# Kernel optimization log

Hardware: AMD Instinct MI355X
Metric: run time of the kernel (lower is better)

The kernel has to match this reference:

```python
import jax, jax.numpy as jnp
import numpy as np

B, E, T, H = 4, 16, 1024, 1024
NEG = -10000.0


def setup_inputs() -> dict:
    key = jax.random.key(0)
    ks = jax.random.split(key, 9)
    s = 1.0 / np.sqrt(H)
    return {
        "token_embedding": jax.random.normal(ks[0], (B, T, H), jnp.float32),
        "entity_embedding": jax.random.normal(ks[1], (B, E, H), jnp.float32),
        "token_mask": jax.random.bernoulli(ks[2], 0.9, (B, T)),
        "Wt": jax.random.normal(ks[3], (H, H), jnp.float32) * s,
        "bt": jax.random.normal(ks[4], (H,), jnp.float32) * s,
        "We": jax.random.normal(ks[5], (H, H), jnp.float32) * s,
        "be": jax.random.normal(ks[6], (H,), jnp.float32) * s,
        "Wp": jax.random.normal(ks[7], (H,), jnp.float32) * s,
        "bp": jax.random.normal(ks[8], (1,), jnp.float32) * s,
    }


def reference(token_embedding, entity_embedding, token_mask, Wt, bt, We, be, Wp, bp):
    # token branch: [B,T,H] @ [H,H] -> [B,T,H]
    t = jnp.einsum('bth,hk->btk', token_embedding, Wt) + bt
    # entity branch: [B,E,H] @ [H,H] -> [B,E,H]
    e = jnp.einsum('beh,hk->bek', entity_embedding, We) + be
    # broadcast add -> relu -> linear-to-scalar: [B,E,T,H] -> [B,E,T]
    m = jax.nn.relu(t[:, None, :, :] + e[:, :, None, :])
    cls = jnp.einsum('beth,h->bet', m, Wp) + bp[0]
    # mask fill (after squeeze, per squeeze=True path)
    cls = jnp.where(token_mask[:, None, :], cls, NEG)
    p = jax.nn.sigmoid(cls)
    return cls, p
```

## Files before the change

### kernel.cpp

```cpp
#include <hip/hip_runtime.h>

typedef unsigned short us;
typedef __attribute__((ext_vector_type(8))) short short8;
typedef __attribute__((ext_vector_type(4))) float f32x4;

__device__ __forceinline__ us f2bf(float f) {
  unsigned int u = __builtin_bit_cast(unsigned int, f);
  u += 0x7fffu + ((u >> 16) & 1u);
  return (us)(u >> 16);
}

__device__ __forceinline__ void gload_lds16(const void* g, void* l) {
  __builtin_amdgcn_global_load_lds(
      (const __attribute__((address_space(1))) void*)g,
      (__attribute__((address_space(3))) void*)l, 16, 0, 0);
}

__global__ __launch_bounds__(256) void prep_kernel(
    const float* __restrict__ token, us* __restrict__ tokb,
    const float* __restrict__ Wt, us* __restrict__ WtT,
    const float* __restrict__ entity, const float* __restrict__ We,
    float* __restrict__ epart) {
  __shared__ float tile[64][65];
  __shared__ float eS[16][128];
  const int bid = blockIdx.x, tid = threadIdx.x;
  if (bid < 256) {
    int kc = bid & 7, nt = (bid >> 3) & 7, b = bid >> 6;
    int k0 = kc << 7, n0 = nt << 7;
#pragma unroll
    for (int p = 0; p < 2; ++p) {
      int idx = (p << 8) + tid;
      int r = idx >> 5, kk = (idx & 31) << 2;
      *(float4*)&eS[r][kk] = *(const float4*)&entity[(size_t)(((b << 4) + r) << 10) + k0 + kk];
    }
    __syncthreads();
    const int col = tid & 127, rh = tid >> 7;
    const float* wP = We + ((size_t)k0 << 10) + n0 + col;
    float acc[8] = {0.f, 0.f, 0.f, 0.f, 0.f, 0.f, 0.f, 0.f};
#pragma unroll 8
    for (int k = 0; k < 128; ++k) {
      float wv = wP[(size_t)k << 10];
#pragma unroll
      for (int r = 0; r < 8; ++r)
        acc[r] = fmaf(wv, eS[(rh << 3) + r][k], acc[r]);
    }
    float* op = epart + (((size_t)((kc << 6) + (b << 4) + (rh << 3))) << 10) + n0 + col;
#pragma unroll
    for (int r = 0; r < 8; ++r) op[(size_t)r << 10] = acc[r];
  } else if (bid < 4352) {
    int q = (bid - 256) * 256 + tid;
    float4 v = ((const float4*)token)[q];
    ushort4 o;
    o.x = f2bf(v.x); o.y = f2bf(v.y); o.z = f2bf(v.z); o.w = f2bf(v.w);
    ((ushort4*)tokb)[q] = o;
  } else {
    int tb = bid - 4352;
    int bx = (tb & 15) << 6, by = ((tb >> 4) & 15) << 6;
    int r0 = tid >> 4, c0 = (tid & 15) << 2;
#pragma unroll
    for (int p = 0; p < 4; ++p) {
      int r = p * 16 + r0;
      float4 v = *(const float4*)&Wt[(size_t)(by + r) * 1024 + bx + c0];
      tile[r][c0] = v.x; tile[r][c0 + 1] = v.y;
      tile[r][c0 + 2] = v.z; tile[r][c0 + 3] = v.w;
    }
    __syncthreads();
#pragma unroll
    for (int p = 0; p < 4; ++p) {
      int r = p * 16 + r0;
      ushort4 o;
      o.x = f2bf(tile[c0 + 0][r]); o.y = f2bf(tile[c0 + 1][r]);
      o.z = f2bf(tile[c0 + 2][r]); o.w = f2bf(tile[c0 + 3][r]);
      *(ushort4*)&WtT[(size_t)(bx + r) * 1024 + by + c0] = o;
    }
  }
}

__global__ __launch_bounds__(256) void main_kernel(
    const us* __restrict__ tokb, const us* __restrict__ WtT,
    const float* __restrict__ epart, const float* __restrict__ be,
    const float* __restrict__ bt, const float* __restrict__ wp,
    float* __restrict__ partial) {
  __shared__ __attribute__((aligned(16))) us Ws[2][4096];
  __shared__ __attribute__((aligned(16))) us Ts[2][2048];
  __shared__ __attribute__((aligned(16))) float eL[16][132];
  __shared__ __attribute__((aligned(16))) float btL[128];
  __shared__ __attribute__((aligned(16))) float wpL[128];
  __shared__ float pp[2][64][17];
  const int tid = threadIdx.x;
  const int mh = blockIdx.x, tt = blockIdx.y;
  const int h0 = mh << 7, b = tt >> 4, t0 = (tt & 15) << 6;
#pragma unroll
  for (int p = 0; p < 2; ++p) {
    int q = (p << 8) + tid;
    int er = q >> 5, ec = (q & 31) << 2;
    f32x4 s = *(const f32x4*)&be[h0 + ec];
#pragma unroll
    for (int kc = 0; kc < 8; ++kc)
      s += *(const f32x4*)&epart[(((size_t)((kc << 6) + (b << 4) + er)) << 10) + h0 + ec];
    *(f32x4*)&eL[er][ec] = s;
  }
  if (tid < 128) btL[tid] = bt[h0 + tid];
  else wpL[tid - 128] = wp[h0 + tid - 128];
  asm volatile("" ::: "memory");
  const int row1 = tid >> 2, kc4 = (tid & 3) << 3;
  const us* wP = WtT + (size_t)(h0 + row1) * 1024 + kc4;
  const us* tP = tokb + (size_t)((b << 10) + t0 + row1) * 1024 + kc4;
  const int w = tid >> 6;
  us* w0 = &Ws[0][w * 512]; us* w1 = &Ws[1][w * 512];
  us* t0L = &Ts[0][w * 512]; us* t1L = &Ts[1][w * 512];
  gload_lds16(wP, w0); gload_lds16(wP + 65536, w0 + 2048);
  gload_lds16(tP, t0L);
  gload_lds16(wP + 32, w1); gload_lds16(wP + 65536 + 32, w1 + 2048);
  gload_lds16(tP + 32, t1L);
  const int lane = tid & 63, wm = (tid >> 7) & 1, wn = (tid >> 6) & 1;
  const int l16 = lane & 15, oct = lane >> 4, ko = oct << 3;
  int wfo[4], tfo[2];
#pragma unroll
  for (int i = 0; i < 4; ++i) wfo[i] = (((wm << 6) + (i << 4) + l16) << 5) + ko;
#pragma unroll
  for (int j = 0; j < 2; ++j) tfo[j] = (((wn << 5) + (j << 4) + l16) << 5) + ko;
  f32x4 acc[4][2] = {};
  for (int kt = 0; kt < 32; ++kt) {
    const us* Wb = Ws[kt & 1];
    const us* Tb = Ts[kt & 1];
    __builtin_amdgcn_s_waitcnt(0x0f73);
    __builtin_amdgcn_s_barrier();
    asm volatile("" ::: "memory");
    short8 af[4], bfr[2];
#pragma unroll
    for (int i = 0; i < 4; ++i) af[i] = *(const short8*)&Wb[wfo[i]];
#pragma unroll
    for (int j = 0; j < 2; ++j) bfr[j] = *(const short8*)&Tb[tfo[j]];
#pragma unroll
    for (int i = 0; i < 4; ++i)
#pragma unroll
      for (int j = 0; j < 2; ++j)
        acc[i][j] = __builtin_amdgcn_mfma_f32_16x16x32_bf16(af[i], bfr[j], acc[i][j], 0, 0, 0);
    asm volatile("" ::: "memory");
    __builtin_amdgcn_s_barrier();
    int nk = kt + 2; if (nk > 31) nk = 30;
    int ko2 = nk << 5;
    us* dw = (kt & 1) ? w1 : w0;
    us* dt = (kt & 1) ? t1L : t0L;
    gload_lds16(wP + ko2, dw); gload_lds16(wP + 65536 + ko2, dw + 2048);
    gload_lds16(tP + ko2, dt);
  }
  f32x4 btq[4], wpq[4];
#pragma unroll
  for (int i = 0; i < 4; ++i) {
    int hb = (wm << 6) + (i << 4) + (oct << 2);
    btq[i] = *(const f32x4*)&btL[hb];
    wpq[i] = *(const f32x4*)&wpL[hb];
  }
#pragma unroll
  for (int i = 0; i < 4; ++i)
#pragma unroll
    for (int j = 0; j < 2; ++j) acc[i][j] += btq[i];
#pragma unroll
  for (int e = 0; e < 16; ++e) {
    f32x4 ev[4];
#pragma unroll
    for (int i = 0; i < 4; ++i)
      ev[i] = *(const f32x4*)&eL[e][(wm << 6) + (i << 4) + (oct << 2)];
    float pj[2] = {0.f, 0.f};
#pragma unroll
    for (int j = 0; j < 2; ++j)
#pragma unroll
      for (int i = 0; i < 4; ++i)
#pragma unroll
        for (int r = 0; r < 4; ++r)
          pj[j] = fmaf(fmaxf(acc[i][j][r] + ev[i][r], 0.f), wpq[i][r], pj[j]);
#pragma unroll
    for (int j = 0; j < 2; ++j) {
      pj[j] += __shfl_xor(pj[j], 16, 64);
      pj[j] += __shfl_xor(pj[j], 32, 64);
    }
    if (oct == 0) {
#pragma unroll
      for (int j = 0; j < 2; ++j) pp[wm][(wn << 5) + (j << 4) + l16][e] = pj[j];
    }
  }
  __syncthreads();
#pragma unroll
  for (int q = 0; q < 4; ++q) {
    int flat = (q << 8) + tid;
    int e = flat >> 6, tl = flat & 63;
    float v = pp[0][tl][e] + pp[1][tl][e];
    partial[((size_t)mh << 16) + (size_t)((((b << 4) + e) << 10) + t0 + tl)] = v;
  }
}

__global__ __launch_bounds__(256) void finalize_kernel(
    const float* __restrict__ partial, const float* __restrict__ bp,
    const int* __restrict__ mask, float* __restrict__ out) {
  int idx = blockIdx.x * 256 + threadIdx.x;
  float s = 0.f;
#pragma unroll
  for (int mh = 0; mh < 8; ++mh) s += partial[((size_t)mh << 16) + idx];
  float cls = s + bp[0];
  int b = idx >> 14, t = idx & 1023;
  if (mask[(b << 10) + t] == 0) cls = -10000.0f;
  float p = 1.0f / (1.0f + __expf(-cls));
  out[idx] = cls;
  out[65536 + idx] = p;
}

extern "C" void kernel_launch(void* const* d_in, const int* in_sizes, int n_in,
                              void* d_out, int out_size, void* d_ws, size_t ws_size,
                              hipStream_t stream) {
  const float* token = (const float*)d_in[0];
  const float* entity = (const float*)d_in[1];
  const int* mask = (const int*)d_in[2];
  const float* Wt = (const float*)d_in[3];
  const float* bt = (const float*)d_in[4];
  const float* We = (const float*)d_in[5];
  const float* be = (const float*)d_in[6];
  const float* Wp = (const float*)d_in[7];
  const float* bp = (const float*)d_in[8];
  float* out = (float*)d_out;

  char* ws = (char*)d_ws;
  us* tokb = (us*)ws;
  us* WtT = tokb + (size_t)4096 * 1024;
  float* epart = (float*)(WtT + (size_t)1024 * 1024);
  float* partial = epart + (size_t)8 * 64 * 1024;

  prep_kernel<<<4608, 256, 0, stream>>>(token, tokb, Wt, WtT, entity, We, epart);
  main_kernel<<<dim3(8, 64), 256, 0, stream>>>(tokb, WtT, epart, be, bt, Wp, partial);
  finalize_kernel<<<256, 256, 0, stream>>>(partial, bp, mask, out);
}
```

Before: 114.0 us.

## Triple-buffer GEMM LDS pipeline and issue prefetch before epilogue setup

Moves the main kernel's K-loop from double to triple buffering, so each tile's global-to-LDS load is issued three steps ahead, and the wait count is relaxed to allow more loads in flight. The first three prefetches are issued before the entity and bias setup so that setup overlaps the memory latency. The epilogue now runs in two halves of eight entities to shrink the partial-sum shared buffer, at the cost of one extra barrier. More LDS per block may reduce occupancy.

```diff
diff --git a/kernel.cpp b/kernel.cpp
--- a/kernel.cpp
+++ b/kernel.cpp
@@ -81,15 +81,27 @@
     const float* __restrict__ epart, const float* __restrict__ be,
     const float* __restrict__ bt, const float* __restrict__ wp,
     float* __restrict__ partial) {
-  __shared__ __attribute__((aligned(16))) us Ws[2][4096];
-  __shared__ __attribute__((aligned(16))) us Ts[2][2048];
+  __shared__ __attribute__((aligned(16))) us Ws[3][4096];
+  __shared__ __attribute__((aligned(16))) us Ts[3][2048];
   __shared__ __attribute__((aligned(16))) float eL[16][132];
   __shared__ __attribute__((aligned(16))) float btL[128];
   __shared__ __attribute__((aligned(16))) float wpL[128];
-  __shared__ float pp[2][64][17];
+  __shared__ float pp[2][64][9];
   const int tid = threadIdx.x;
   const int mh = blockIdx.x, tt = blockIdx.y;
   const int h0 = mh << 7, b = tt >> 4, t0 = (tt & 15) << 6;
+  const int row1 = tid >> 2, kc4 = (tid & 3) << 3;
+  const us* wP = WtT + (size_t)(h0 + row1) * 1024 + kc4;
+  const us* tP = tokb + (size_t)((b << 10) + t0 + row1) * 1024 + kc4;
+  const int w = tid >> 6;
+  us* wB[3] = {&Ws[0][w * 512], &Ws[1][w * 512], &Ws[2][w * 512]};
+  us* tB[3] = {&Ts[0][w * 512], &Ts[1][w * 512], &Ts[2][w * 512]};
+#pragma unroll
+  for (int j = 0; j < 3; ++j) {
+    gload_lds16(wP + (j << 5), wB[j]);
+    gload_lds16(wP + 65536 + (j << 5), wB[j] + 2048);
+    gload_lds16(tP + (j << 5), tB[j]);
+  }
 #pragma unroll
   for (int p = 0; p < 2; ++p) {
     int q = (p << 8) + tid;
@@ -103,16 +115,6 @@
   if (tid < 128) btL[tid] = bt[h0 + tid];
   else wpL[tid - 128] = wp[h0 + tid - 128];
   asm volatile("" ::: "memory");
-  const int row1 = tid >> 2, kc4 = (tid & 3) << 3;
-  const us* wP = WtT + (size_t)(h0 + row1) * 1024 + kc4;
-  const us* tP = tokb + (size_t)((b << 10) + t0 + row1) * 1024 + kc4;
-  const int w = tid >> 6;
-  us* w0 = &Ws[0][w * 512]; us* w1 = &Ws[1][w * 512];
-  us* t0L = &Ts[0][w * 512]; us* t1L = &Ts[1][w * 512];
-  gload_lds16(wP, w0); gload_lds16(wP + 65536, w0 + 2048);
-  gload_lds16(tP, t0L);
-  gload_lds16(wP + 32, w1); gload_lds16(wP + 65536 + 32, w1 + 2048);
-  gload_lds16(tP + 32, t1L);
   const int lane = tid & 63, wm = (tid >> 7) & 1, wn = (tid >> 6) & 1;
   const int l16 = lane & 15, oct = lane >> 4, ko = oct << 3;
   int wfo[4], tfo[2];
@@ -121,31 +123,39 @@
 #pragma unroll
   for (int j = 0; j < 2; ++j) tfo[j] = (((wn << 5) + (j << 4) + l16) << 5) + ko;
   f32x4 acc[4][2] = {};
-  for (int kt = 0; kt < 32; ++kt) {
-    const us* Wb = Ws[kt & 1];
-    const us* Tb = Ts[kt & 1];
-    __builtin_amdgcn_s_waitcnt(0x0f73);
-    __builtin_amdgcn_s_barrier();
-    asm volatile("" ::: "memory");
-    short8 af[4], bfr[2];
-#pragma unroll
-    for (int i = 0; i < 4; ++i) af[i] = *(const short8*)&Wb[wfo[i]];
-#pragma unroll
-    for (int j = 0; j < 2; ++j) bfr[j] = *(const short8*)&Tb[tfo[j]];
-#pragma unroll
-    for (int i = 0; i < 4; ++i)
-#pragma unroll
-      for (int j = 0; j < 2; ++j)
-        acc[i][j] = __builtin_amdgcn_mfma_f32_16x16x32_bf16(af[i], bfr[j], acc[i][j], 0, 0, 0);
-    asm volatile("" ::: "memory");
-    __builtin_amdgcn_s_barrier();
-    int nk = kt + 2; if (nk > 31) nk = 30;
-    int ko2 = nk << 5;
-    us* dw = (kt & 1) ? w1 : w0;
-    us* dt = (kt & 1) ? t1L : t0L;
-    gload_lds16(wP + ko2, dw); gload_lds16(wP + 65536 + ko2, dw + 2048);
-    gload_lds16(tP + ko2, dt);
-  }
+#define KBODY(KT, BUF, VMC, ISSUE)                                              \
+  {                                                                             \
+    __builtin_amdgcn_s_waitcnt(VMC);                                            \
+    __builtin_amdgcn_s_barrier();                                               \
+    asm volatile("" ::: "memory");                                              \
+    short8 af[4], bfr[2];                                                       \
+    _Pragma("unroll") for (int i = 0; i < 4; ++i)                               \
+        af[i] = *(const short8*)&Ws[BUF][wfo[i]];                               \
+    _Pragma("unroll") for (int j = 0; j < 2; ++j)                               \
+        bfr[j] = *(const short8*)&Ts[BUF][tfo[j]];                              \
+    _Pragma("unroll") for (int i = 0; i < 4; ++i)                               \
+        _Pragma("unroll") for (int j = 0; j < 2; ++j)                           \
+            acc[i][j] = __builtin_amdgcn_mfma_f32_16x16x32_bf16(                \
+                af[i], bfr[j], acc[i][j], 0, 0, 0);                             \
+    asm volatile("" ::: "memory");                                              \
+    if (ISSUE) {                                                                \
+      __builtin_amdgcn_s_barrier();                                             \
+      int nk = (KT) + 3; if (nk > 31) nk = 31;  \
+      int ko2 = nk << 5;                                                        \
+      gload_lds16(wP + ko2, wB[BUF]);                                           \
+      gload_lds16(wP + 65536 + ko2, wB[BUF] + 2048);                            \
+      gload_lds16(tP + ko2, tB[BUF]);                                           \
+    }                                                                           \
+  }
+  for (int g = 0; g < 10; ++g) {
+    int kt = g * 3;
+    KBODY(kt + 0, 0, 0x0f76, 1);
+    KBODY(kt + 1, 1, 0x0f76, 1);
+    KBODY(kt + 2, 2, 0x0f76, 1);
+  }
+  KBODY(30, 0, 0x0f76, 0);
+  KBODY(31, 1, 0x0f73, 0);
+#undef KBODY
   f32x4 btq[4], wpq[4];
 #pragma unroll
   for (int i = 0; i < 4; ++i) {
@@ -157,37 +167,42 @@
   for (int i = 0; i < 4; ++i)
 #pragma unroll
     for (int j = 0; j < 2; ++j) acc[i][j] += btq[i];
-#pragma unroll
-  for (int e = 0; e < 16; ++e) {
-    f32x4 ev[4];
-#pragma unroll
-    for (int i = 0; i < 4; ++i)
-      ev[i] = *(const f32x4*)&eL[e][(wm << 6) + (i << 4) + (oct << 2)];
-    float pj[2] = {0.f, 0.f};
-#pragma unroll
-    for (int j = 0; j < 2; ++j)
+  for (int eh = 0; eh < 2; ++eh) {
+    __syncthreads();
+#pragma unroll
+    for (int e8 = 0; e8 < 8; ++e8) {
+      int e = (eh << 3) + e8;
+      f32x4 ev[4];
 #pragma unroll
       for (int i = 0; i < 4; ++i)
-#pragma unroll
-        for (int r = 0; r < 4; ++r)
-          pj[j] = fmaf(fmaxf(acc[i][j][r] + ev[i][r], 0.f), wpq[i][r], pj[j]);
-#pragma unroll
-    for (int j = 0; j < 2; ++j) {
-      pj[j] += __shfl_xor(pj[j], 16, 64);
-      pj[j] += __shfl_xor(pj[j], 32, 64);
-    }
-    if (oct == 0) {
-#pragma unroll
-      for (int j = 0; j < 2; ++j) pp[wm][(wn << 5) + (j << 4) + l16][e] = pj[j];
-    }
-  }
-  __syncthreads();
-#pragma unroll
-  for (int q = 0; q < 4; ++q) {
-    int flat = (q << 8) + tid;
-    int e = flat >> 6, tl = flat & 63;
-    float v = pp[0][tl][e] + pp[1][tl][e];
-    partial[((size_t)mh << 16) + (size_t)((((b << 4) + e) << 10) + t0 + tl)] = v;
+        ev[i] = *(const f32x4*)&eL[e][(wm << 6) + (i << 4) + (oct << 2)];
+      float pj[2] = {0.f, 0.f};
+#pragma unroll
+      for (int j = 0; j < 2; ++j)
+#pragma unroll
+        for (int i = 0; i < 4; ++i)
+#pragma unroll
+          for (int r = 0; r < 4; ++r)
+            pj[j] = fmaf(fmaxf(acc[i][j][r] + ev[i][r], 0.f), wpq[i][r], pj[j]);
+#pragma unroll
+      for (int j = 0; j < 2; ++j) {
+        pj[j] += __shfl_xor(pj[j], 16, 64);
+        pj[j] += __shfl_xor(pj[j], 32, 64);
+      }
+      if (oct == 0) {
+#pragma unroll
+        for (int j = 0; j < 2; ++j) pp[wm][(wn << 5) + (j << 4) + l16][e8] = pj[j];
+      }
+    }
+    __syncthreads();
+#pragma unroll
+    for (int q = 0; q < 2; ++q) {
+      int flat = (q << 8) + tid;
+      int e8 = flat >> 6, tl = flat & 63;
+      float v = pp[0][tl][e8] + pp[1][tl][e8];
+      partial[((size_t)mh << 16) +
+              (size_t)((((b << 4) + (eh << 3) + e8) << 10) + t0 + tl)] = v;
+    }
   }
 }
 
```

Result: no change. 114.9 us (+0.8%).

## Fuse finalize into main kernel via atomic counter, load GEMM operands directly

Applied to the files above, without the earlier changes.

Removes the finalize kernel launch: each main-kernel block increments a per-token-tile counter, and the last of the 8 hidden-slice blocks sums the partials and writes cls and sigmoid outputs. The LDS double-buffered global_load_lds pipeline is replaced by direct per-lane global loads of MFMA fragments, with no per-step barriers. The grid is transposed and the pp scratch halved to 8 entities per pass. This saves a launch and the barrier overhead, but it gives up LDS staging and coalesced tile loads, so global load efficiency and latency hiding may suffer.

```diff
diff --git a/kernel.cpp b/kernel.cpp
--- a/kernel.cpp
+++ b/kernel.cpp
@@ -10,20 +10,15 @@
   return (us)(u >> 16);
 }
 
-__device__ __forceinline__ void gload_lds16(const void* g, void* l) {
-  __builtin_amdgcn_global_load_lds(
-      (const __attribute__((address_space(1))) void*)g,
-      (__attribute__((address_space(3))) void*)l, 16, 0, 0);
-}
-
 __global__ __launch_bounds__(256) void prep_kernel(
     const float* __restrict__ token, us* __restrict__ tokb,
     const float* __restrict__ Wt, us* __restrict__ WtT,
     const float* __restrict__ entity, const float* __restrict__ We,
-    float* __restrict__ epart) {
+    float* __restrict__ epart, int* __restrict__ cnt) {
   __shared__ float tile[64][65];
   __shared__ float eS[16][128];
   const int bid = blockIdx.x, tid = threadIdx.x;
+  if (bid == 0 && tid < 64) cnt[tid] = 0;
   if (bid < 256) {
     int kc = bid & 7, nt = (bid >> 3) & 7, b = bid >> 6;
     int k0 = kc << 7, n0 = nt << 7;
@@ -80,15 +75,16 @@
     const us* __restrict__ tokb, const us* __restrict__ WtT,
     const float* __restrict__ epart, const float* __restrict__ be,
     const float* __restrict__ bt, const float* __restrict__ wp,
-    float* __restrict__ partial) {
-  __shared__ __attribute__((aligned(16))) us Ws[2][4096];
-  __shared__ __attribute__((aligned(16))) us Ts[2][2048];
+    const float* __restrict__ bp, const int* __restrict__ mask,
+    float* __restrict__ partial, int* __restrict__ cnt,
+    float* __restrict__ out) {
   __shared__ __attribute__((aligned(16))) float eL[16][132];
   __shared__ __attribute__((aligned(16))) float btL[128];
   __shared__ __attribute__((aligned(16))) float wpL[128];
-  __shared__ float pp[2][64][17];
+  __shared__ float pp[2][64][9];
+  __shared__ int doneFlag;
   const int tid = threadIdx.x;
-  const int mh = blockIdx.x, tt = blockIdx.y;
+  const int tt = blockIdx.x, mh = blockIdx.y;
   const int h0 = mh << 7, b = tt >> 4, t0 = (tt & 15) << 6;
 #pragma unroll
   for (int p = 0; p < 2; ++p) {
@@ -102,50 +98,32 @@
   }
   if (tid < 128) btL[tid] = bt[h0 + tid];
   else wpL[tid - 128] = wp[h0 + tid - 128];
-  asm volatile("" ::: "memory");
-  const int row1 = tid >> 2, kc4 = (tid & 3) << 3;
-  const us* wP = WtT + (size_t)(h0 + row1) * 1024 + kc4;
-  const us* tP = tokb + (size_t)((b << 10) + t0 + row1) * 1024 + kc4;
-  const int w = tid >> 6;
-  us* w0 = &Ws[0][w * 512]; us* w1 = &Ws[1][w * 512];
-  us* t0L = &Ts[0][w * 512]; us* t1L = &Ts[1][w * 512];
-  gload_lds16(wP, w0); gload_lds16(wP + 65536, w0 + 2048);
-  gload_lds16(tP, t0L);
-  gload_lds16(wP + 32, w1); gload_lds16(wP + 65536 + 32, w1 + 2048);
-  gload_lds16(tP + 32, t1L);
   const int lane = tid & 63, wm = (tid >> 7) & 1, wn = (tid >> 6) & 1;
-  const int l16 = lane & 15, oct = lane >> 4, ko = oct << 3;
-  int wfo[4], tfo[2];
-#pragma unroll
-  for (int i = 0; i < 4; ++i) wfo[i] = (((wm << 6) + (i << 4) + l16) << 5) + ko;
-#pragma unroll
-  for (int j = 0; j < 2; ++j) tfo[j] = (((wn << 5) + (j << 4) + l16) << 5) + ko;
+  const int l16 = lane & 15, oct = lane >> 4;
+  const us* aP[4];
+  const us* bP[2];
+#pragma unroll
+  for (int i = 0; i < 4; ++i)
+    aP[i] = WtT + (size_t)(h0 + (wm << 6) + (i << 4) + l16) * 1024 + (oct << 3);
+#pragma unroll
+  for (int j = 0; j < 2; ++j)
+    bP[j] = tokb + (size_t)((b << 10) + t0 + (wn << 5) + (j << 4) + l16) * 1024 + (oct << 3);
   f32x4 acc[4][2] = {};
+#pragma unroll 4
   for (int kt = 0; kt < 32; ++kt) {
-    const us* Wb = Ws[kt & 1];
-    const us* Tb = Ts[kt & 1];
-    __builtin_amdgcn_s_waitcnt(0x0f73);
-    __builtin_amdgcn_s_barrier();
-    asm volatile("" ::: "memory");
+    const int ko = kt << 5;
     short8 af[4], bfr[2];
 #pragma unroll
-    for (int i = 0; i < 4; ++i) af[i] = *(const short8*)&Wb[wfo[i]];
-#pragma unroll
-    for (int j = 0; j < 2; ++j) bfr[j] = *(const short8*)&Tb[tfo[j]];
+    for (int i = 0; i < 4; ++i) af[i] = *(const short8*)(aP[i] + ko);
+#pragma unroll
+    for (int j = 0; j < 2; ++j) bfr[j] = *(const short8*)(bP[j] + ko);
 #pragma unroll
     for (int i = 0; i < 4; ++i)
 #pragma unroll
       for (int j = 0; j < 2; ++j)
         acc[i][j] = __builtin_amdgcn_mfma_f32_16x16x32_bf16(af[i], bfr[j], acc[i][j], 0, 0, 0);
-    asm volatile("" ::: "memory");
-    __builtin_amdgcn_s_barrier();
-    int nk = kt + 2; if (nk > 31) nk = 30;
-    int ko2 = nk << 5;
-    us* dw = (kt & 1) ? w1 : w0;
-    us* dt = (kt & 1) ? t1L : t0L;
-    gload_lds16(wP + ko2, dw); gload_lds16(wP + 65536 + ko2, dw + 2048);
-    gload_lds16(tP + ko2, dt);
-  }
+  }
+  __syncthreads();
   f32x4 btq[4], wpq[4];
 #pragma unroll
   for (int i = 0; i < 4; ++i) {
@@ -157,53 +135,66 @@
   for (int i = 0; i < 4; ++i)
 #pragma unroll
     for (int j = 0; j < 2; ++j) acc[i][j] += btq[i];
-#pragma unroll
-  for (int e = 0; e < 16; ++e) {
-    f32x4 ev[4];
-#pragma unroll
-    for (int i = 0; i < 4; ++i)
-      ev[i] = *(const f32x4*)&eL[e][(wm << 6) + (i << 4) + (oct << 2)];
-    float pj[2] = {0.f, 0.f};
-#pragma unroll
-    for (int j = 0; j < 2; ++j)
+  for (int eh = 0; eh < 2; ++eh) {
+    __syncthreads();
+#pragma unroll
+    for (int e8 = 0; e8 < 8; ++e8) {
+      int e = (eh << 3) + e8;
+      f32x4 ev[4];
 #pragma unroll
       for (int i = 0; i < 4; ++i)
-#pragma unroll
-        for (int r = 0; r < 4; ++r)
-          pj[j] = fmaf(fmaxf(acc[i][j][r] + ev[i][r], 0.f), wpq[i][r], pj[j]);
-#pragma unroll
-    for (int j = 0; j < 2; ++j) {
-      pj[j] += __shfl_xor(pj[j], 16, 64);
-      pj[j] += __shfl_xor(pj[j], 32, 64);
-    }
-    if (oct == 0) {
-#pragma unroll
-      for (int j = 0; j < 2; ++j) pp[wm][(wn << 5) + (j << 4) + l16][e] = pj[j];
-    }
+        ev[i] = *(const f32x4*)&eL[e][(wm << 6) + (i << 4) + (oct << 2)];
+      float pj[2] = {0.f, 0.f};
+#pragma unroll
+      for (int j = 0; j < 2; ++j)
+#pragma unroll
+        for (int i = 0; i < 4; ++i)
+#pragma unroll
+          for (int r = 0; r < 4; ++r)
+            pj[j] = fmaf(fmaxf(acc[i][j][r] + ev[i][r], 0.f), wpq[i][r], pj[j]);
+#pragma unroll
+      for (int j = 0; j < 2; ++j) {
+        pj[j] += __shfl_xor(pj[j], 16, 64);
+        pj[j] += __shfl_xor(pj[j], 32, 64);
+      }
+      if (oct == 0) {
+#pragma unroll
+        for (int j = 0; j < 2; ++j) pp[wm][(wn << 5) + (j << 4) + l16][e8] = pj[j];
+      }
+    }
+    __syncthreads();
+#pragma unroll
+    for (int q = 0; q < 2; ++q) {
+      int flat = (q << 8) + tid;
+      int e8 = flat >> 6, tl = flat & 63;
+      float v = pp[0][tl][e8] + pp[1][tl][e8];
+      partial[((size_t)mh << 16) +
+              (size_t)((((b << 4) + (eh << 3) + e8) << 10) + t0 + tl)] = v;
+    }
+  }
+  __threadfence();
+  if (tid == 0) {
+    int old = atomicAdd(cnt + tt, 1);
+    doneFlag = (old == 7);
   }
   __syncthreads();
-#pragma unroll
-  for (int q = 0; q < 4; ++q) {
-    int flat = (q << 8) + tid;
-    int e = flat >> 6, tl = flat & 63;
-    float v = pp[0][tl][e] + pp[1][tl][e];
-    partial[((size_t)mh << 16) + (size_t)((((b << 4) + e) << 10) + t0 + tl)] = v;
-  }
-}
-
-__global__ __launch_bounds__(256) void finalize_kernel(
-    const float* __restrict__ partial, const float* __restrict__ bp,
-    const int* __restrict__ mask, float* __restrict__ out) {
-  int idx = blockIdx.x * 256 + threadIdx.x;
-  float s = 0.f;
-#pragma unroll
-  for (int mh = 0; mh < 8; ++mh) s += partial[((size_t)mh << 16) + idx];
-  float cls = s + bp[0];
-  int b = idx >> 14, t = idx & 1023;
-  if (mask[(b << 10) + t] == 0) cls = -10000.0f;
-  float p = 1.0f / (1.0f + __expf(-cls));
-  out[idx] = cls;
-  out[65536 + idx] = p;
+  if (doneFlag) {
+    __threadfence();
+#pragma unroll
+    for (int q = 0; q < 4; ++q) {
+      int flat = (q << 8) + tid;
+      int e = flat >> 6, tl = flat & 63;
+      int t = t0 + tl;
+      size_t oidx = ((size_t)((b << 4) + e) << 10) + t;
+      float s = 0.f;
+#pragma unroll
+      for (int m = 0; m < 8; ++m) s += partial[((size_t)m << 16) + oidx];
+      float cls = s + bp[0];
+      if (mask[(b << 10) + t] == 0) cls = -10000.0f;
+      out[oidx] = cls;
+      out[65536 + oidx] = 1.0f / (1.0f + __expf(-cls));
+    }
+  }
 }
 
 extern "C" void kernel_launch(void* const* d_in, const int* in_sizes, int n_in,
@@ -225,8 +216,9 @@
   us* WtT = tokb + (size_t)4096 * 1024;
   float* epart = (float*)(WtT + (size_t)1024 * 1024);
   float* partial = epart + (size_t)8 * 64 * 1024;
-
-  prep_kernel<<<4608, 256, 0, stream>>>(token, tokb, Wt, WtT, entity, We, epart);
-  main_kernel<<<dim3(8, 64), 256, 0, stream>>>(tokb, WtT, epart, be, bt, Wp, partial);
-  finalize_kernel<<<256, 256, 0, stream>>>(partial, bp, mask, out);
-}
+  int* cnt = (int*)(partial + (size_t)8 * 64 * 1024);
+
+  prep_kernel<<<4608, 256, 0, stream>>>(token, tokb, Wt, WtT, entity, We, epart, cnt);
+  main_kernel<<<dim3(64, 8), 256, 0, stream>>>(tokb, WtT, epart, be, bt, Wp, bp, mask,
+                                               partial, cnt, out);
+}
```

After: 176.3 us. 1.55x slower.
